# Kernel optimization log

Hardware: AMD Instinct MI355X
Metric: run time of the kernel (lower is better)

The kernel has to match this reference:

```python
import jax, jax.numpy as jnp
import numpy as np
import math

L, D, H, DK, DFF, B, S = 4, 512, 8, 256, 2048, 8, 256
HD = H * DK
EPS = 1e-6


def _norm(x, alpha, bias):
    # torch: alpha*(x-mean)/(std_unbiased + eps) + bias  (std uses ddof=1)
    mu = x.mean(axis=-1, keepdims=True)
    var = ((x - mu) ** 2).sum(axis=-1, keepdims=True) / (x.shape[-1] - 1)
    return alpha * (x - mu) / (jnp.sqrt(var) + EPS) + bias


def _positional_encoding():
    pos = jnp.arange(S, dtype=jnp.float32)[:, None]          # [S,1]
    i = jnp.arange(0, D, 2, dtype=jnp.float32)               # even indices
    pe_sin = jnp.sin(pos / (S ** (2.0 * i / D)))             # [S,D/2]
    pe_cos = jnp.cos(pos / (S ** (2.0 * (i + 1.0) / D)))     # [S,D/2]
    pe = jnp.zeros((S, D), dtype=jnp.float32)
    pe = pe.at[:, 0::2].set(pe_sin).at[:, 1::2].set(pe_cos)
    return pe


def setup_inputs() -> dict:
    key = jax.random.key(0)
    ks = jax.random.split(key, 16)
    sc = 0.02
    inp = {
        "data": jax.random.normal(ks[0], (B, S, D), dtype=jnp.float32),
        "attn_m": jax.random.randint(ks[1], (B, S), 0, 2, dtype=jnp.int32),
        "view_idx": 0,
        "seg_emb": jax.random.normal(ks[2], (3, D), dtype=jnp.float32) * sc,
        "Wq": jax.random.normal(ks[3], (L, D, HD), dtype=jnp.float32) * sc,
        "bq": jnp.zeros((L, HD), dtype=jnp.float32),
        "Wk": jax.random.normal(ks[4], (L, D, HD), dtype=jnp.float32) * sc,
        "bk": jnp.zeros((L, HD), dtype=jnp.float32),
        "Wv": jax.random.normal(ks[5], (L, D, HD), dtype=jnp.float32) * sc,
        "bv": jnp.zeros((L, HD), dtype=jnp.float32),
        "Wo": jax.random.normal(ks[6], (L, HD, D), dtype=jnp.float32) * sc,
        "bo": jnp.zeros((L, D), dtype=jnp.float32),
        "W1": jax.random.normal(ks[7], (L, D, DFF), dtype=jnp.float32) * sc,
        "b1": jnp.zeros((L, DFF), dtype=jnp.float32),
        "W2": jax.random.normal(ks[8], (L, DFF, D), dtype=jnp.float32) * sc,
        "b2": jnp.zeros((L, D), dtype=jnp.float32),
        "alpha1": jnp.ones((L, D), dtype=jnp.float32),
        "bias1": jnp.zeros((L, D), dtype=jnp.float32),
        "alpha2": jnp.ones((L, D), dtype=jnp.float32),
        "bias2": jnp.zeros((L, D), dtype=jnp.float32),
        "alpha_f": jnp.ones((D,), dtype=jnp.float32),
        "bias_f": jnp.zeros((D,), dtype=jnp.float32),
    }
    return inp


def reference(data, attn_m, view_idx, seg_emb, Wq, bq, Wk, bk, Wv, bv, Wo, bo,
              W1, b1, W2, b2, alpha1, bias1, alpha2, bias2, alpha_f, bias_f):
    # positional encoder: x*sqrt(d_f) + pe + seg_embedding(view_idx*seq_len)
    pe = _positional_encoding()
    seg_idx = view_idx * S  # scalar; must be < 3 (view_idx == 0 in practice)
    x = data * math.sqrt(D) + pe[None, :, :] + seg_emb[seg_idx][None, None, :]

    # mask: attn_m [B,S] -> [B,1,1,S] bool, True = masked (key axis)
    maskb = attn_m.astype(bool)[:, None, None, :]

    for i in range(L):
        x2 = _norm(x, alpha1[i], bias1[i])
        q = (x2 @ Wq[i] + bq[i]).reshape(B, S, H, DK).transpose(0, 2, 1, 3)
        k = (x2 @ Wk[i] + bk[i]).reshape(B, S, H, DK).transpose(0, 2, 1, 3)
        v = (x2 @ Wv[i] + bv[i]).reshape(B, S, H, DK).transpose(0, 2, 1, 3)
        scores = jnp.einsum('bhqd,bhkd->bhqk', q, k) / math.sqrt(DK)
        scores = jnp.where(maskb, -1e9, scores)
        attnw = jax.nn.softmax(scores, axis=-1)
        o = jnp.einsum('bhqk,bhkd->bhqd', attnw, v)
        o = o.transpose(0, 2, 1, 3).reshape(B, S, HD) @ Wo[i] + bo[i]
        x = x + o
        x2 = _norm(x, alpha2[i], bias2[i])
        ff = jax.nn.relu(x2 @ W1[i] + b1[i]) @ W2[i] + b2[i]
        x = x + ff

    return _norm(x, alpha_f, bias_f)
```

## Files before the change

### kernel.cpp

```cpp
#include <hip/hip_runtime.h>
#include <hip/hip_bf16.h>

#define LNUM 4
#define DIM  512
#define SS   256

typedef unsigned short ushort_t;
typedef __attribute__((ext_vector_type(8))) short bf16x8;
typedef __attribute__((ext_vector_type(4))) float f32x4;
typedef __attribute__((ext_vector_type(8))) unsigned short u16x8;

#define VWAIT(n) asm volatile("s_waitcnt vmcnt(" #n ")" ::: "memory")
__device__ __forceinline__ void bar() { __builtin_amdgcn_s_barrier(); }

__device__ __forceinline__ ushort_t f2b(float f) {
  union { float f; unsigned u; } x; x.f = f;
  unsigned r = x.u + 0x7FFFu + ((x.u >> 16) & 1u);
  return (ushort_t)(r >> 16);
}

__device__ __forceinline__ void gload16(const void* g, void* s) {
  __builtin_amdgcn_global_load_lds((const __attribute__((address_space(1))) void*)g,
                                   (__attribute__((address_space(3))) void*)s, 16, 0, 0);
}

template<int TM, int TN, int EPI>
__global__ __launch_bounds__(256, 2)
void gemm_bt(const ushort_t* __restrict__ A, const ushort_t* __restrict__ B,
             const float* __restrict__ bias, const float* __restrict__ bias2,
             const float* __restrict__ bias3,
             ushort_t* __restrict__ outB, ushort_t* __restrict__ outB2,
             ushort_t* __restrict__ outB3, float* __restrict__ outF,
             int K, int lda, int ldb, int ldc, int nkz, int relu,
             long zA, long zB)
{
  constexpr int CA = TM / 32, CB = TN / 32, SN = CA + CB;
  constexpr int WM = TM / 32, WN = TN / 32;
  constexpr bool BATCH = (EPI == 4);
  __shared__ ushort_t As[3 * TM * 64];
  __shared__ ushort_t Bs[3 * TN * 64];
  const int tid = threadIdx.x, lane = tid & 63, wid = tid >> 6;
  const int wm = wid >> 1, wn = wid & 1;
  const int z = blockIdx.z;
  const int kz = BATCH ? 0 : z;
  const int Kz = K / nkz, k0 = kz * Kz, nt = Kz >> 6;

  const ushort_t* Ab = A + (BATCH ? (long)z * zA : 0) + (long)blockIdx.y * TM * lda + k0;
  const ushort_t* Bb = B + (BATCH ? (long)z * zB : 0) + (long)blockIdx.x * TN * ldb + k0;

  const ushort_t* srcA[CA]; ushort_t* ldsA[CA];
  const ushort_t* srcB[CB]; ushort_t* ldsB[CB];
#pragma unroll
  for (int c = 0; c < CA; ++c) {
    int off = c * 4096 + tid * 16;
    int row = off >> 7;
    int scol = ((off & 127) ^ ((row & 7) << 4)) >> 1;
    srcA[c] = Ab + (long)row * lda + scol;
    ldsA[c] = As + c * 2048 + wid * 512;
  }
#pragma unroll
  for (int c = 0; c < CB; ++c) {
    int off = c * 4096 + tid * 16;
    int row = off >> 7;
    int scol = ((off & 127) ^ ((row & 7) << 4)) >> 1;
    srcB[c] = Bb + (long)row * ldb + scol;
    ldsB[c] = Bs + c * 2048 + wid * 512;
  }

  f32x4 acc[WM][WN] = {};

  auto STAGE = [&](int buf, int t) {
#pragma unroll
    for (int c = 0; c < CA; ++c) gload16(srcA[c] + t * 64, ldsA[c] + buf * TM * 64);
#pragma unroll
    for (int c = 0; c < CB; ++c) gload16(srcB[c] + t * 64, ldsB[c] + buf * TN * 64);
  };

  STAGE(0, 0);
  STAGE(1, 1);
  for (int t = 0; t < nt; ++t) {
    if (t < nt - 1) { if constexpr (SN == 6) VWAIT(6); else VWAIT(4); }
    else VWAIT(0);
    bar();
    if (t + 2 < nt) STAGE((t + 2) % 3, t + 2);
    const int buf = t % 3;
#pragma unroll
    for (int ks = 0; ks < 2; ++ks) {
      const int kb = ks * 64 + ((lane >> 4) << 4);
      bf16x8 af[WM], bfr[WN];
#pragma unroll
      for (int f = 0; f < WM; ++f) {
        int ra = wm * (TM / 2) + f * 16 + (lane & 15);
        af[f] = *(const bf16x8*)((const char*)As + buf * TM * 128 + ra * 128 + (kb ^ ((ra & 7) << 4)));
      }
#pragma unroll
      for (int g = 0; g < WN; ++g) {
        int rb = wn * (TN / 2) + g * 16 + (lane & 15);
        bfr[g] = *(const bf16x8*)((const char*)Bs + buf * TN * 128 + rb * 128 + (kb ^ ((rb & 7) << 4)));
      }
      __builtin_amdgcn_s_setprio(1);
#pragma unroll
      for (int i = 0; i < WM; ++i)
#pragma unroll
        for (int j = 0; j < WN; ++j)
          acc[i][j] = __builtin_amdgcn_mfma_f32_16x16x32_bf16(af[i], bfr[j], acc[i][j], 0, 0, 0);
      __builtin_amdgcn_s_setprio(0);
    }
  }

  const int row0 = blockIdx.y * TM + wm * (TM / 2) + ((lane >> 4) << 2);
  int col0 = blockIdx.x * TN + wn * (TN / 2) + (lane & 15);
  const float* bsel = bias;
  ushort_t* osel = outB;
  int seg = 0;
  if (EPI == 3) {
    seg = (blockIdx.x * TN) >> 11;
    if (seg == 1) { bsel = bias2; osel = outB2; }
    else if (seg == 2) { bsel = bias3; }
    col0 -= seg * 2048;
  }

  if (EPI == 3 && seg == 2) {
    ushort_t* Vt = As;
    bar();
#pragma unroll
    for (int i = 0; i < WM; ++i)
#pragma unroll
      for (int j = 0; j < WN; ++j) {
        const int colL = wn * (TN / 2) + j * 16 + (lane & 15);
        const float bv = bsel[(col0 + j * 16) & 2047];
#pragma unroll
        for (int r = 0; r < 4; ++r) {
          const int rowL = wm * (TM / 2) + i * 16 + ((lane >> 4) << 2) + r;
          Vt[colL * 136 + rowL] = f2b(acc[i][j][r] + bv);
        }
      }
    bar();
    const int colvBase = blockIdx.x * TN - 4096;
    const int h = colvBase >> 8, dk0 = colvBase & 255;
    const int rowBase = blockIdx.y * TM;
    const int bh = ((rowBase >> 8) << 3) + h;
    const int s0 = rowBase & 255;
    const int dkl = tid >> 2, scc = (tid & 3) * 32;
    ushort_t* dst = outB3 + ((long)bh << 16) + (long)(dk0 + dkl) * 256 + s0 + scc;
#pragma unroll
    for (int m = 0; m < 4; ++m)
      *(u16x8*)(dst + m * 8) = *(const u16x8*)(Vt + dkl * 136 + scc + m * 8);
    return;
  }

#pragma unroll
  for (int i = 0; i < WM; ++i) {
#pragma unroll
    for (int j = 0; j < WN; ++j) {
      const int col = col0 + j * 16;
      float bv = 0.f;
      if (EPI == 2) bv = (kz == 0) ? bias[col] : 0.f;
      else if (EPI == 0 || EPI == 3) bv = bsel[col];
#pragma unroll
      for (int r = 0; r < 4; ++r) {
        const int row = row0 + i * 16 + r;
        float v = acc[i][j][r] + bv;
        if (EPI == 2) {
          outF[(long)kz * 1048576 + (long)row * ldc + col] = v;
        } else if (EPI == 3) {
          const long addr = (((long)(row >> 8) * 8 + (col >> 8)) << 16) +
                            (long)(row & 255) * 256 + (col & 255);
          osel[addr] = f2b(v);
        } else if (EPI == 4) {
          const int bb = z >> 3, hh = z & 7;
          osel[(long)(bb * 256 + row) * 2048 + hh * 256 + col] = f2b(acc[i][j][r]);
        } else {
          if (relu) v = fmaxf(v, 0.f);
          osel[(long)row * ldc + col] = f2b(v);
        }
      }
    }
  }
}

__global__ __launch_bounds__(256, 2)
void scoresm_k(const ushort_t* __restrict__ qh, const ushort_t* __restrict__ kh,
               const int* __restrict__ attnm, ushort_t* __restrict__ P)
{
  __shared__ ushort_t As[2][64 * 64];
  __shared__ ushort_t Bs[2][256 * 64];
  const int bh = blockIdx.x, qt = blockIdx.y;
  const int b = bh >> 3;
  const int tid = threadIdx.x, lane = tid & 63, wid = tid >> 6;
  const int l15 = lane & 15, l4 = lane >> 4;

  unsigned mbits = 0;
#pragma unroll
  for (int j = 0; j < 16; ++j)
    mbits |= (attnm[b * 256 + j * 16 + l15] != 0 ? 1u : 0u) << j;

  const ushort_t* Qb = qh + ((long)bh << 16) + qt * 64 * 256;
  const ushort_t* Kb = kh + ((long)bh << 16);
  const ushort_t* srcA[2]; ushort_t* ldsA[2];
  const ushort_t* srcB[8]; ushort_t* ldsB[8];
#pragma unroll
  for (int c = 0; c < 2; ++c) {
    int off = c * 4096 + tid * 16;
    int row = off >> 7;
    int scol = ((off & 127) ^ ((row & 7) << 4)) >> 1;
    srcA[c] = Qb + (long)row * 256 + scol;
    ldsA[c] = As[0] + c * 2048 + wid * 512;
  }
#pragma unroll
  for (int c = 0; c < 8; ++c) {
    int off = c * 4096 + tid * 16;
    int row = off >> 7;
    int scol = ((off & 127) ^ ((row & 7) << 4)) >> 1;
    srcB[c] = Kb + (long)row * 256 + scol;
    ldsB[c] = Bs[0] + c * 2048 + wid * 512;
  }

  auto STAGE = [&](int buf, int t) {
#pragma unroll
    for (int c = 0; c < 2; ++c) gload16(srcA[c] + t * 64, ldsA[c] + buf * 4096);
#pragma unroll
    for (int c = 0; c < 8; ++c) gload16(srcB[c] + t * 64, ldsB[c] + buf * 16384);
  };

  f32x4 sacc[16] = {};
  STAGE(0, 0);
  for (int t = 0; t < 4; ++t) {
    VWAIT(0);
    bar();
    if (t < 3) STAGE((t + 1) & 1, t + 1);
    const int buf = t & 1;
#pragma unroll
    for (int ks = 0; ks < 2; ++ks) {
      const int kb = ks * 64 + (l4 << 4);
      const int ra = wid * 16 + l15;
      bf16x8 af = *(const bf16x8*)((const char*)As[buf] + ra * 128 + (kb ^ ((ra & 7) << 4)));
      __builtin_amdgcn_s_setprio(1);
#pragma unroll
      for (int j = 0; j < 16; ++j) {
        const int rb = j * 16 + l15;
        bf16x8 bf_ = *(const bf16x8*)((const char*)Bs[buf] + rb * 128 + (kb ^ ((rb & 7) << 4)));
        sacc[j] = __builtin_amdgcn_mfma_f32_16x16x32_bf16(af, bf_, sacc[j], 0, 0, 0);
      }
      __builtin_amdgcn_s_setprio(0);
    }
  }

  float mr[4] = {-3e38f, -3e38f, -3e38f, -3e38f}, sr[4] = {};
#pragma unroll
  for (int j = 0; j < 16; ++j) {
    const bool mk = (mbits >> j) & 1;
#pragma unroll
    for (int r = 0; r < 4; ++r) {
      float s = mk ? -1e9f : sacc[j][r] * 0.0625f;
      sacc[j][r] = s;
      mr[r] = fmaxf(mr[r], s);
    }
  }
#pragma unroll
  for (int o = 1; o < 16; o <<= 1)
#pragma unroll
    for (int r = 0; r < 4; ++r) mr[r] = fmaxf(mr[r], __shfl_xor(mr[r], o, 16));
#pragma unroll
  for (int j = 0; j < 16; ++j)
#pragma unroll
    for (int r = 0; r < 4; ++r) {
      float e = __expf(sacc[j][r] - mr[r]);
      sacc[j][r] = e;
      sr[r] += e;
    }
#pragma unroll
  for (int o = 1; o < 16; o <<= 1)
#pragma unroll
    for (int r = 0; r < 4; ++r) sr[r] += __shfl_xor(sr[r], o, 16);
#pragma unroll
  for (int r = 0; r < 4; ++r) sr[r] = 1.f / sr[r];

  ushort_t* Rp = (ushort_t*)Bs;
  bar();
#pragma unroll
  for (int j = 0; j < 16; ++j)
#pragma unroll
    for (int r = 0; r < 4; ++r) {
      const int row = wid * 16 + l4 * 4 + r;
      *(ushort_t*)((char*)Rp + row * 512 + (((j * 16 + l15) * 2) ^ ((row & 7) << 4))) =
          f2b(sacc[j][r] * sr[r]);
    }
  bar();
  const int row = tid >> 2, cb0 = (tid & 3) * 128;
  ushort_t* dst = P + ((long)bh << 16) + (long)(qt * 64 + row) * 256 + (cb0 >> 1);
#pragma unroll
  for (int m = 0; m < 8; ++m) {
    u16x8 v = *(const u16x8*)((const char*)Rp + row * 512 + ((cb0 + m * 16) ^ ((row & 7) << 4)));
    *(u16x8*)(dst + m * 8) = v;
  }
}

__global__ __launch_bounds__(256)
void build_x(const float* __restrict__ data, const float* __restrict__ seg,
             const int* __restrict__ viewp, float* __restrict__ x)
{
  int i = blockIdx.x * 256 + threadIdx.x;
  int d = i & 511;
  int s = (i >> 9) & 255;
  float ang = (float)s * exp2f((float)d * -0.03125f);
  float pe = (d & 1) ? cosf(ang) : sinf(ang);
  int vrow = viewp[0] * SS;
  x[i] = data[i] * 22.627416997969522f + pe + seg[vrow * DIM + d];
}

__global__ __launch_bounds__(256)
void lnorm_k(const float* __restrict__ x, const float* __restrict__ parts, int np,
             float* __restrict__ xout,
             const float* __restrict__ alpha, const float* __restrict__ beta,
             ushort_t* __restrict__ outB, float* __restrict__ outF)
{
  const int row = blockIdx.x, tid = threadIdx.x;
  const long base = (long)row * DIM;
  float2 v = ((const float2*)(x + base))[tid];
  if (np) {
    for (int p = 0; p < np; ++p) {
      float2 a = ((const float2*)(parts + (long)p * 1048576 + base))[tid];
      v.x += a.x; v.y += a.y;
    }
    ((float2*)(xout + base))[tid] = v;
  }
  float s = v.x + v.y;
#pragma unroll
  for (int o = 32; o; o >>= 1) s += __shfl_xor(s, o, 64);
  __shared__ float rs[4], rq[4];
  if ((tid & 63) == 0) rs[tid >> 6] = s;
  __syncthreads();
  const float mu = (rs[0] + rs[1] + rs[2] + rs[3]) * (1.f / 512.f);
  const float dx = v.x - mu, dy = v.y - mu;
  float q = dx * dx + dy * dy;
#pragma unroll
  for (int o = 32; o; o >>= 1) q += __shfl_xor(q, o, 64);
  if ((tid & 63) == 0) rq[tid >> 6] = q;
  __syncthreads();
  const float var = (rq[0] + rq[1] + rq[2] + rq[3]) * (1.f / 511.f);
  const float rstd = 1.f / (sqrtf(var) + 1e-6f);
  const int d0 = tid * 2;
  const float o0 = alpha[d0] * dx * rstd + beta[d0];
  const float o1 = alpha[d0 + 1] * dy * rstd + beta[d0 + 1];
  if (outB) { outB[base + d0] = f2b(o0); outB[base + d0 + 1] = f2b(o1); }
  else      { outF[base + d0] = o0;      outF[base + d0 + 1] = o1; }
}

__global__ __launch_bounds__(256)
void wtrans(const float* __restrict__ in, ushort_t* __restrict__ out,
             int R, int C, long ozs)
{
  __shared__ float t[32][33];
  const int z = blockIdx.z;
  const long zi = (long)z * R * C, zo = (long)z * ozs;
  const int c0 = blockIdx.x * 32, r0 = blockIdx.y * 32;
  const int tx = threadIdx.x & 31, ty = threadIdx.x >> 5;
#pragma unroll
  for (int i = 0; i < 4; ++i) t[ty + i * 8][tx] = in[zi + (long)(r0 + ty + i * 8) * C + c0 + tx];
  __syncthreads();
#pragma unroll
  for (int i = 0; i < 4; ++i) out[zo + (long)(c0 + ty + i * 8) * R + r0 + tx] = f2b(t[tx][ty + i * 8]);
}

extern "C" void kernel_launch(void* const* d_in, const int* in_sizes, int n_in,
                              void* d_out, int out_size, void* d_ws, size_t ws_size,
                              hipStream_t stream)
{
  const float* data  = (const float*)d_in[0];
  const int*   attnm = (const int*)d_in[1];
  const int*   viewp = (const int*)d_in[2];
  const float* seg   = (const float*)d_in[3];
  const float* Wq    = (const float*)d_in[4];
  const float* bq    = (const float*)d_in[5];
  const float* Wk    = (const float*)d_in[6];
  const float* bk    = (const float*)d_in[7];
  const float* Wv    = (const float*)d_in[8];
  const float* bv    = (const float*)d_in[9];
  const float* Wo    = (const float*)d_in[10];
  const float* bo    = (const float*)d_in[11];
  const float* W1    = (const float*)d_in[12];
  const float* b1    = (const float*)d_in[13];
  const float* W2    = (const float*)d_in[14];
  const float* b2    = (const float*)d_in[15];
  const float* al1   = (const float*)d_in[16];
  const float* be1   = (const float*)d_in[17];
  const float* al2   = (const float*)d_in[18];
  const float* be2   = (const float*)d_in[19];
  const float* alf   = (const float*)d_in[20];
  const float* bef   = (const float*)d_in[21];

  char* w = (char*)d_ws;
  const size_t MB = 1024 * 1024;
  ushort_t* qkvW = (ushort_t*)(w + 0 * MB);
  ushort_t* WoT  = (ushort_t*)(w + 24 * MB);
  ushort_t* W1T  = (ushort_t*)(w + 32 * MB);
  ushort_t* W2T  = (ushort_t*)(w + 40 * MB);
  float*    x    = (float*)   (w + 48 * MB);
  ushort_t* x2   = (ushort_t*)(w + 52 * MB);
  ushort_t* qb   = (ushort_t*)(w + 54 * MB);
  ushort_t* kbf  = (ushort_t*)(w + 62 * MB);
  ushort_t* vT   = (ushort_t*)(w + 70 * MB);
  ushort_t* ao   = (ushort_t*)(w + 78 * MB);
  ushort_t* ffh  = (ushort_t*)(w + 86 * MB);
  float*    parts= (float*)   (w + 94 * MB);
  ushort_t* P    = (ushort_t*)(w + 110 * MB);

  dim3 blk(256);
  const long QKV_L = 6144L * 512;
  wtrans<<<dim3(64, 16, 4), blk, 0, stream>>>(Wq, qkvW + 0 * 2048 * 512, 512, 2048, QKV_L);
  wtrans<<<dim3(64, 16, 4), blk, 0, stream>>>(Wk, qkvW + 1 * 2048 * 512, 512, 2048, QKV_L);
  wtrans<<<dim3(64, 16, 4), blk, 0, stream>>>(Wv, qkvW + 2 * 2048 * 512, 512, 2048, QKV_L);
  wtrans<<<dim3(16, 64, 4), blk, 0, stream>>>(Wo, WoT, 2048, 512, 512L * 2048);
  wtrans<<<dim3(64, 16, 4), blk, 0, stream>>>(W1, W1T, 512, 2048, 2048L * 512);
  wtrans<<<dim3(16, 64, 4), blk, 0, stream>>>(W2, W2T, 2048, 512, 512L * 2048);
  build_x<<<4096, blk, 0, stream>>>(data, seg, viewp, x);

  for (int i = 0; i < LNUM; ++i) {
    if (i == 0)
      lnorm_k<<<2048, blk, 0, stream>>>(x, nullptr, 0, nullptr, al1, be1, x2, nullptr);
    gemm_bt<128, 64, 3><<<dim3(96, 16, 1), blk, 0, stream>>>(
        x2, qkvW + (long)i * QKV_L, bq + i * 2048, bk + i * 2048, bv + i * 2048,
        qb, kbf, vT, nullptr, 512, 512, 512, 2048, 1, 0, 0, 0);
    scoresm_k<<<dim3(64, 4), blk, 0, stream>>>(qb, kbf, attnm, P);
    gemm_bt<128, 64, 4><<<dim3(4, 2, 64), blk, 0, stream>>>(
        P, vT, nullptr, nullptr, nullptr,
        ao, nullptr, nullptr, nullptr, 256, 256, 256, 2048, 1, 0,
        65536, 65536);
    gemm_bt<64, 64, 2><<<dim3(8, 32, 2), blk, 0, stream>>>(
        ao, WoT + (long)i * 512 * 2048, bo + i * 512, nullptr, nullptr,
        nullptr, nullptr, nullptr, parts, 2048, 2048, 2048, 512, 2, 0, 0, 0);
    lnorm_k<<<2048, blk, 0, stream>>>(x, parts, 2, x, al2 + i * 512, be2 + i * 512, x2, nullptr);
    gemm_bt<128, 64, 0><<<dim3(32, 16, 1), blk, 0, stream>>>(
        x2, W1T + (long)i * 2048 * 512, b1 + i * 2048, nullptr, nullptr,
        ffh, nullptr, nullptr, nullptr, 512, 512, 512, 2048, 1, 1, 0, 0);
    gemm_bt<64, 64, 2><<<dim3(8, 32, 2), blk, 0, stream>>>(
        ffh, W2T + (long)i * 512 * 2048, b2 + i * 512, nullptr, nullptr,
        nullptr, nullptr, nullptr, parts, 2048, 2048, 2048, 512, 2, 0, 0, 0);
    if (i < LNUM - 1)
      lnorm_k<<<2048, blk, 0, stream>>>(x, parts, 2, x, al1 + (i + 1) * 512, be1 + (i + 1) * 512, x2, nullptr);
    else
      lnorm_k<<<2048, blk, 0, stream>>>(x, parts, 2, x, alf, bef, nullptr, (float*)d_out);
  }
}
```

Baseline: 447.3 us.

## Use 128x128 double-buffered tiles for QKV GEMM and merge weight transposes

Switches the fused QKV projection GEMM from 128x64 triple-buffered tiles to 128x128 tiles with a two-stage LDS buffer. This improves operand reuse and halves the grid, and the smaller buffer count keeps LDS usage in bounds. The V-transpose epilogue is rewritten to stage the wider tile through LDS in two halves. The six weight-transpose launches are merged into two kernels to cut launch overhead. The cost is a shallower prefetch pipeline (wait-all each iteration) and fewer blocks for the QKV GEMM.

```diff
diff --git a/kernel.cpp b/kernel.cpp
--- a/kernel.cpp
+++ b/kernel.cpp
@@ -24,7 +24,7 @@
                                    (__attribute__((address_space(3))) void*)s, 16, 0, 0);
 }
 
-template<int TM, int TN, int EPI>
+template<int TM, int TN, int EPI, int NBUF>
 __global__ __launch_bounds__(256, 2)
 void gemm_bt(const ushort_t* __restrict__ A, const ushort_t* __restrict__ B,
              const float* __restrict__ bias, const float* __restrict__ bias2,
@@ -37,8 +37,8 @@
   constexpr int CA = TM / 32, CB = TN / 32, SN = CA + CB;
   constexpr int WM = TM / 32, WN = TN / 32;
   constexpr bool BATCH = (EPI == 4);
-  __shared__ ushort_t As[3 * TM * 64];
-  __shared__ ushort_t Bs[3 * TN * 64];
+  __shared__ ushort_t As[NBUF * TM * 64];
+  __shared__ ushort_t Bs[NBUF * TN * 64];
   const int tid = threadIdx.x, lane = tid & 63, wid = tid >> 6;
   const int wm = wid >> 1, wn = wid & 1;
   const int z = blockIdx.z;
@@ -76,14 +76,7 @@
     for (int c = 0; c < CB; ++c) gload16(srcB[c] + t * 64, ldsB[c] + buf * TN * 64);
   };
 
-  STAGE(0, 0);
-  STAGE(1, 1);
-  for (int t = 0; t < nt; ++t) {
-    if (t < nt - 1) { if constexpr (SN == 6) VWAIT(6); else VWAIT(4); }
-    else VWAIT(0);
-    bar();
-    if (t + 2 < nt) STAGE((t + 2) % 3, t + 2);
-    const int buf = t % 3;
+  auto COMPUTE = [&](int buf) {
 #pragma unroll
     for (int ks = 0; ks < 2; ++ks) {
       const int kb = ks * 64 + ((lane >> 4) << 4);
@@ -105,6 +98,25 @@
         for (int j = 0; j < WN; ++j)
           acc[i][j] = __builtin_amdgcn_mfma_f32_16x16x32_bf16(af[i], bfr[j], acc[i][j], 0, 0, 0);
       __builtin_amdgcn_s_setprio(0);
+    }
+  };
+
+  STAGE(0, 0);
+  if constexpr (NBUF == 3) {
+    STAGE(1, 1);
+    for (int t = 0; t < nt; ++t) {
+      if (t < nt - 1) { if constexpr (SN == 6) VWAIT(6); else VWAIT(4); }
+      else VWAIT(0);
+      bar();
+      if (t + 2 < nt) STAGE((t + 2) % 3, t + 2);
+      COMPUTE(t % 3);
+    }
+  } else {
+    for (int t = 0; t < nt; ++t) {
+      VWAIT(0);
+      bar();
+      if (t + 1 < nt) STAGE((t + 1) & 1, t + 1);
+      COMPUTE(t & 1);
     }
   }
 
@@ -122,30 +134,58 @@
 
   if (EPI == 3 && seg == 2) {
     ushort_t* Vt = As;
-    bar();
-#pragma unroll
-    for (int i = 0; i < WM; ++i)
-#pragma unroll
-      for (int j = 0; j < WN; ++j) {
-        const int colL = wn * (TN / 2) + j * 16 + (lane & 15);
-        const float bv = bsel[(col0 + j * 16) & 2047];
-#pragma unroll
-        for (int r = 0; r < 4; ++r) {
-          const int rowL = wm * (TM / 2) + i * 16 + ((lane >> 4) << 2) + r;
-          Vt[colL * 136 + rowL] = f2b(acc[i][j][r] + bv);
-        }
-      }
-    bar();
     const int colvBase = blockIdx.x * TN - 4096;
+    const int rowBase = blockIdx.y * TM;
     const int h = colvBase >> 8, dk0 = colvBase & 255;
-    const int rowBase = blockIdx.y * TM;
     const int bh = ((rowBase >> 8) << 3) + h;
     const int s0 = rowBase & 255;
-    const int dkl = tid >> 2, scc = (tid & 3) * 32;
-    ushort_t* dst = outB3 + ((long)bh << 16) + (long)(dk0 + dkl) * 256 + s0 + scc;
-#pragma unroll
-    for (int m = 0; m < 4; ++m)
-      *(u16x8*)(dst + m * 8) = *(const u16x8*)(Vt + dkl * 136 + scc + m * 8);
+    bar();
+    if constexpr (TN == 64) {
+#pragma unroll
+      for (int i = 0; i < WM; ++i)
+#pragma unroll
+        for (int j = 0; j < WN; ++j) {
+          const int colL = wn * (TN / 2) + j * 16 + (lane & 15);
+          const float bv = bsel[col0 + j * 16];
+#pragma unroll
+          for (int r = 0; r < 4; ++r) {
+            const int rowL = wm * (TM / 2) + i * 16 + ((lane >> 4) << 2) + r;
+            Vt[colL * 136 + rowL] = f2b(acc[i][j][r] + bv);
+          }
+        }
+      bar();
+      const int dkl = tid >> 2, scc = (tid & 3) * 32;
+      ushort_t* dst = outB3 + ((long)bh << 16) + (long)(dk0 + dkl) * 256 + s0 + scc;
+#pragma unroll
+      for (int m = 0; m < 4; ++m)
+        *(u16x8*)(dst + m * 8) = *(const u16x8*)(Vt + dkl * 136 + scc + m * 8);
+    } else {
+#pragma unroll
+      for (int half = 0; half < 2; ++half) {
+        if (half) bar();
+        if (wn == half) {
+#pragma unroll
+          for (int i = 0; i < WM; ++i)
+#pragma unroll
+            for (int j = 0; j < WN; ++j) {
+              const int colL = j * 16 + (lane & 15);
+              const float bv = bsel[col0 + j * 16];
+#pragma unroll
+              for (int r = 0; r < 4; ++r) {
+                const int rowL = wm * 64 + i * 16 + ((lane >> 4) << 2) + r;
+                Vt[colL * 136 + rowL] = f2b(acc[i][j][r] + bv);
+              }
+            }
+        }
+        bar();
+        const int dkl = tid >> 2, scc = (tid & 3) * 32;
+        ushort_t* dst = outB3 + ((long)bh << 16) +
+                        (long)(dk0 + half * 64 + dkl) * 256 + s0 + scc;
+#pragma unroll
+        for (int m = 0; m < 4; ++m)
+          *(u16x8*)(dst + m * 8) = *(const u16x8*)(Vt + dkl * 136 + scc + m * 8);
+      }
+    }
     return;
   }
 
@@ -348,19 +388,40 @@
 }
 
 __global__ __launch_bounds__(256)
-void wtrans(const float* __restrict__ in, ushort_t* __restrict__ out,
-             int R, int C, long ozs)
+void wtransA(const float* __restrict__ Wq, const float* __restrict__ Wk,
+             const float* __restrict__ Wv, const float* __restrict__ W1,
+             ushort_t* __restrict__ qkvW, ushort_t* __restrict__ W1T)
 {
   __shared__ float t[32][33];
-  const int z = blockIdx.z;
-  const long zi = (long)z * R * C, zo = (long)z * ozs;
+  const int z = blockIdx.z, widx = z >> 2, layer = z & 3;
+  const float* src = (widx == 0) ? Wq : (widx == 1) ? Wk : (widx == 2) ? Wv : W1;
+  src += (long)layer * 512 * 2048;
+  ushort_t* dst = (widx == 3) ? (W1T + (long)layer * 2048 * 512)
+                              : (qkvW + (long)layer * (6144L * 512) + (long)widx * 2048 * 512);
   const int c0 = blockIdx.x * 32, r0 = blockIdx.y * 32;
   const int tx = threadIdx.x & 31, ty = threadIdx.x >> 5;
 #pragma unroll
-  for (int i = 0; i < 4; ++i) t[ty + i * 8][tx] = in[zi + (long)(r0 + ty + i * 8) * C + c0 + tx];
+  for (int i = 0; i < 4; ++i) t[ty + i * 8][tx] = src[(long)(r0 + ty + i * 8) * 2048 + c0 + tx];
   __syncthreads();
 #pragma unroll
-  for (int i = 0; i < 4; ++i) out[zo + (long)(c0 + ty + i * 8) * R + r0 + tx] = f2b(t[tx][ty + i * 8]);
+  for (int i = 0; i < 4; ++i) dst[(long)(c0 + ty + i * 8) * 512 + r0 + tx] = f2b(t[tx][ty + i * 8]);
+}
+
+__global__ __launch_bounds__(256)
+void wtransB(const float* __restrict__ Wo, const float* __restrict__ W2,
+             ushort_t* __restrict__ WoT, ushort_t* __restrict__ W2T)
+{
+  __shared__ float t[32][33];
+  const int z = blockIdx.z, widx = z >> 2, layer = z & 3;
+  const float* src = ((widx == 0) ? Wo : W2) + (long)layer * 2048 * 512;
+  ushort_t* dst = ((widx == 0) ? WoT : W2T) + (long)layer * 512 * 2048;
+  const int c0 = blockIdx.x * 32, r0 = blockIdx.y * 32;
+  const int tx = threadIdx.x & 31, ty = threadIdx.x >> 5;
+#pragma unroll
+  for (int i = 0; i < 4; ++i) t[ty + i * 8][tx] = src[(long)(r0 + ty + i * 8) * 512 + c0 + tx];
+  __syncthreads();
+#pragma unroll
+  for (int i = 0; i < 4; ++i) dst[(long)(c0 + ty + i * 8) * 2048 + r0 + tx] = f2b(t[tx][ty + i * 8]);
 }
 
 extern "C" void kernel_launch(void* const* d_in, const int* in_sizes, int n_in,
@@ -408,33 +469,29 @@
 
   dim3 blk(256);
   const long QKV_L = 6144L * 512;
-  wtrans<<<dim3(64, 16, 4), blk, 0, stream>>>(Wq, qkvW + 0 * 2048 * 512, 512, 2048, QKV_L);
-  wtrans<<<dim3(64, 16, 4), blk, 0, stream>>>(Wk, qkvW + 1 * 2048 * 512, 512, 2048, QKV_L);
-  wtrans<<<dim3(64, 16, 4), blk, 0, stream>>>(Wv, qkvW + 2 * 2048 * 512, 512, 2048, QKV_L);
-  wtrans<<<dim3(16, 64, 4), blk, 0, stream>>>(Wo, WoT, 2048, 512, 512L * 2048);
-  wtrans<<<dim3(64, 16, 4), blk, 0, stream>>>(W1, W1T, 512, 2048, 2048L * 512);
-  wtrans<<<dim3(16, 64, 4), blk, 0, stream>>>(W2, W2T, 2048, 512, 512L * 2048);
+  wtransA<<<dim3(64, 16, 16), blk, 0, stream>>>(Wq, Wk, Wv, W1, qkvW, W1T);
+  wtransB<<<dim3(16, 64, 8), blk, 0, stream>>>(Wo, W2, WoT, W2T);
   build_x<<<4096, blk, 0, stream>>>(data, seg, viewp, x);
 
   for (int i = 0; i < LNUM; ++i) {
     if (i == 0)
       lnorm_k<<<2048, blk, 0, stream>>>(x, nullptr, 0, nullptr, al1, be1, x2, nullptr);
-    gemm_bt<128, 64, 3><<<dim3(96, 16, 1), blk, 0, stream>>>(
+    gemm_bt<128, 128, 3, 2><<<dim3(48, 16, 1), blk, 0, stream>>>(
         x2, qkvW + (long)i * QKV_L, bq + i * 2048, bk + i * 2048, bv + i * 2048,
         qb, kbf, vT, nullptr, 512, 512, 512, 2048, 1, 0, 0, 0);
     scoresm_k<<<dim3(64, 4), blk, 0, stream>>>(qb, kbf, attnm, P);
-    gemm_bt<128, 64, 4><<<dim3(4, 2, 64), blk, 0, stream>>>(
+    gemm_bt<128, 64, 4, 3><<<dim3(4, 2, 64), blk, 0, stream>>>(
         P, vT, nullptr, nullptr, nullptr,
         ao, nullptr, nullptr, nullptr, 256, 256, 256, 2048, 1, 0,
         65536, 65536);
-    gemm_bt<64, 64, 2><<<dim3(8, 32, 2), blk, 0, stream>>>(
+    gemm_bt<64, 64, 2, 3><<<dim3(8, 32, 2), blk, 0, stream>>>(
         ao, WoT + (long)i * 512 * 2048, bo + i * 512, nullptr, nullptr,
         nullptr, nullptr, nullptr, parts, 2048, 2048, 2048, 512, 2, 0, 0, 0);
     lnorm_k<<<2048, blk, 0, stream>>>(x, parts, 2, x, al2 + i * 512, be2 + i * 512, x2, nullptr);
-    gemm_bt<128, 64, 0><<<dim3(32, 16, 1), blk, 0, stream>>>(
+    gemm_bt<128, 64, 0, 3><<<dim3(32, 16, 1), blk, 0, stream>>>(
         x2, W1T + (long)i * 2048 * 512, b1 + i * 2048, nullptr, nullptr,
         ffh, nullptr, nullptr, nullptr, 512, 512, 512, 2048, 1, 1, 0, 0);
-    gemm_bt<64, 64, 2><<<dim3(8, 32, 2), blk, 0, stream>>>(
+    gemm_bt<64, 64, 2, 3><<<dim3(8, 32, 2), blk, 0, stream>>>(
         ffh, W2T + (long)i * 512 * 2048, b2 + i * 512, nullptr, nullptr,
         nullptr, nullptr, nullptr, parts, 2048, 2048, 2048, 512, 2, 0, 0, 0);
     if (i < LNUM - 1)
```

Result: faster. 431.4 us (median of 2 runs) (-3.5%).
